# Performance work log

Hardware: AMD Instinct MI355X
Metric: run time of the kernel (lower is better)

The kernel has to match this reference:

```python
import jax, jax.numpy as jnp
import numpy as np


def setup_inputs() -> dict:
    key = jax.random.key(0)
    k1, k2 = jax.random.split(key)
    B, T = 16, 2048
    n_fft = 1024
    hop_length = 256
    win_length = 1024
    N = n_fft // 2 + 1  # 513 rfft bins
    spec_real = jax.random.normal(k1, (B, N, T), dtype=jnp.float32)
    spec_imag = jax.random.normal(k2, (B, N, T), dtype=jnp.float32)
    # periodic Hann window (torch.hann_window default)
    n = jnp.arange(win_length, dtype=jnp.float32)
    window = 0.5 * (1.0 - jnp.cos(2.0 * jnp.pi * n / win_length))
    return {
        "spec_real": spec_real,
        "spec_imag": spec_imag,
        "window": window,
        "n_fft": n_fft,
        "hop_length": hop_length,
        "win_length": win_length,
    }


def reference(spec_real, spec_imag, window, n_fft, hop_length, win_length):
    pad = (win_length - hop_length) // 2
    B, N, T = spec_real.shape
    spec = spec_real + 1j * spec_imag  # [B, N, T] complex
    # irfft along freq dim with 'backward' norm (jnp default): [B, n_fft, T]
    ifft = jnp.fft.irfft(spec, n=n_fft, axis=1)
    ifft = ifft * window[None, :, None]  # windowed frames
    L = (T - 1) * hop_length + win_length  # overlap-add output length
    # scatter indices: sample positions of each frame, shape [win_length, T]
    idx = jnp.arange(T)[None, :] * hop_length + jnp.arange(win_length)[:, None]
    y = jnp.zeros((B, L), dtype=ifft.dtype).at[:, idx].add(ifft)
    y = y[:, pad:L - pad]
    # window-squared envelope, same overlap-add pattern
    wsq = jnp.broadcast_to((window * window)[:, None], (win_length, T))
    env = jnp.zeros((L,), dtype=window.dtype).at[idx].add(wsq)[pad:L - pad]
    return y / env
```

## Files before the change

kernel.cpp:

```cpp
#include <hip/hip_runtime.h>

#define BB 16
#define TT 2048
#define NROW 513
#define HOP 256
#define OUTLB 524288
#define FTO 28
#define SPAN (FTO*HOP)
#define TILES 74
#define NCH 4
#define RZ 513

__device__ __forceinline__ int brev9(int k){ return (int)(__brev((unsigned)k)>>23); }
__device__ __forceinline__ int zidx(int f,int m){ return f*RZ + (m ^ ((m>>4)&28) ^ (f<<2)); }

__global__ __launch_bounds__(256,2) void istft_fused(
    const float* __restrict__ sr, const float* __restrict__ si,
    float* __restrict__ out)
{
  __shared__ float2 zc[8*RZ];
  __shared__ __align__(16) float2 ola[SPAN/2];
  __shared__ float2 ttab[256];

  const int tid  = threadIdx.x;
  const int b    = blockIdx.x / TILES;
  const int tile = blockIdx.x % TILES;
  const int L0   = tile*SPAN + 384;
  const int Tbase= tile*FTO - 2;

  { float s,c; __sincosf((float)tid*0.012271846303085130f,&s,&c); ttab[tid]=make_float2(c,s); }
  for (int i=tid;i<SPAN/2;i+=256) ola[i]=make_float2(0.f,0.f);

  const int f  = tid & 7;
  const int pp = tid >> 3;
  const float* srb = sr + (size_t)b*NROW*TT;
  const float* sib = si + (size_t)b*NROW*TT;

  for (int c = 0; c < NCH; ++c) {
    const int t  = Tbase + 8*c + f;
    const int tc = min(max(t,0),TT-1);
    const float msk = (t>=0 && t<TT) ? 1.f : 0.f;
    __syncthreads();

    for (int cc=0; cc<8; ++cc) {
      int k = cc*32 + pp;
      float ar = srb[(size_t)k*TT + tc]*msk;
      float ai = sib[(size_t)k*TT + tc]*msk;
      float br = srb[(size_t)(512-k)*TT + tc]*msk;
      float bi = sib[(size_t)(512-k)*TT + tc]*msk;
      if (k==0) {
        zc[zidx(f,0)] = make_float2(0.5f*(ar+br), 0.5f*(ar-br));
        float cr = srb[(size_t)256*TT + tc]*msk;
        float ci = sib[(size_t)256*TT + tc]*msk;
        zc[zidx(f,1)] = make_float2(cr,-ci);
      } else {
        float st,ct; __sincosf((float)k*0.006135923151542565f,&st,&ct);
        float Er=0.5f*(ar+br), Ei=0.5f*(ai-bi);
        float Dr=0.5f*(ar-br), Di=0.5f*(ai+bi);
        float Or=Dr*ct-Di*st,  Oi=Dr*st+Di*ct;
        zc[zidx(f,brev9(k))]     = make_float2(Er-Oi, Ei+Or);
        zc[zidx(f,brev9(512-k))] = make_float2(Er+Oi, Or-Ei);
      }
    }

    for (int st=0; st<4; ++st) {
      __syncthreads();
      const int h = 1<<(2*st);
      #pragma unroll
      for (int i=0;i<4;++i) {
        int q   = pp + 32*i;
        int ilo = q & (h-1);
        int base= ((q>>(2*st))<<(2*st+2)) + ilo;
        float2 w1 = ttab[ilo<<(8-2*st)];
        float2 w2 = ttab[ilo<<(7-2*st)];
        float2 e0=zc[zidx(f,base)],     e1=zc[zidx(f,base+h)];
        float2 e2=zc[zidx(f,base+2*h)], e3=zc[zidx(f,base+3*h)];
        float t1r=e1.x*w1.x-e1.y*w1.y, t1i=e1.x*w1.y+e1.y*w1.x;
        float t3r=e3.x*w1.x-e3.y*w1.y, t3i=e3.x*w1.y+e3.y*w1.x;
        float arr=e0.x+t1r, ari=e0.y+t1i, brr=e0.x-t1r, bri=e0.y-t1i;
        float crr=e2.x+t3r, cri=e2.y+t3i, drr=e2.x-t3r, dri=e2.y-t3i;
        float cwr=crr*w2.x-cri*w2.y, cwi=crr*w2.y+cri*w2.x;
        float dwr=drr*w2.x-dri*w2.y, dwi=drr*w2.y+dri*w2.x;
        zc[zidx(f,base)]     = make_float2(arr+cwr, ari+cwi);
        zc[zidx(f,base+2*h)] = make_float2(arr-cwr, ari-cwi);
        zc[zidx(f,base+h)]   = make_float2(brr-dwi, bri+dwr);
        zc[zidx(f,base+3*h)] = make_float2(brr+dwi, bri-dwr);
      }
    }
    __syncthreads();
    #pragma unroll
    for (int i=0;i<8;++i) {
      int q = pp + 32*i;
      float2 tw = ttab[q];
      float2 u = zc[zidx(f,q)], v = zc[zidx(f,q+256)];
      float tr=v.x*tw.x-v.y*tw.y, ti=v.x*tw.y+v.y*tw.x;
      zc[zidx(f,q)]     = make_float2(u.x+tr, u.y+ti);
      zc[zidx(f,q+256)] = make_float2(u.x-tr, u.y-ti);
    }

    for (int g=0; g<4; ++g) {
      __syncthreads();
      int slot = g + 4*(tid>>7);
      int tg   = Tbase + 8*c + slot;
      int offB = tg*HOP - L0;
      bool vt  = (tg>=0 && tg<TT);
      int mb   = tid & 127;
      #pragma unroll
      for (int i=0;i<4;++i) {
        int m = mb + 128*i;
        float2 v = zc[zidx(slot,m)];
        int j0 = 2*m;
        float w0 = 0.5f-0.5f*__cosf((float)j0    *0.006135923151542565f);
        float w1v= 0.5f-0.5f*__cosf((float)(j0+1)*0.006135923151542565f);
        int idx = offB + j0;
        if (vt && idx>=0 && idx<SPAN) {
          float2 o = ola[idx>>1];
          o.x += v.x*(1.f/512.f)*w0;
          o.y += v.y*(1.f/512.f)*w1v;
          ola[idx>>1] = o;
        }
      }
    }
  }
  __syncthreads();

  const bool edge = (tile==0)|(tile==TILES-1);
  float* outb = out + (size_t)b*OUTLB;
  for (int i=0;i<7;++i) {
    int i4 = tid + 256*i;
    int s  = 4*i4;
    int gs = tile*SPAN + s;
    if (gs < OUTLB) {
      float4 v = ((const float4*)ola)[i4];
      float r[4]={v.x,v.y,v.z,v.w};
      if (!edge) {
        #pragma unroll
        for(int e=0;e<4;++e) r[e] *= (2.f/3.f);
      } else {
        #pragma unroll
        for(int e=0;e<4;++e) {
          int l = L0 + s + e;
          int j0 = l & 255, tb = l >> 8;
          float env=0.f;
          #pragma unroll
          for (int mm=0;mm<4;++mm) {
            int t2 = tb-mm;
            if (t2>=0 && t2<TT) {
              float wv = 0.5f-0.5f*__cosf((float)(j0+256*mm)*0.006135923151542565f);
              env += wv*wv;
            }
          }
          r[e] /= env;
        }
      }
      *(float4*)(outb+gs) = make_float4(r[0],r[1],r[2],r[3]);
    }
  }
}

extern "C" void kernel_launch(void* const* d_in, const int* in_sizes, int n_in,
                              void* d_out, int out_size, void* d_ws, size_t ws_size,
                              hipStream_t stream) {
  const float* sr = (const float*)d_in[0];
  const float* si = (const float*)d_in[1];
  float* out = (float*)d_out;
  istft_fused<<<BB*TILES, 256, 0, stream>>>(sr, si, out);
}
```

Measured before the change: 260.1 us.

## Double block size and prefetch both frame chunks' spectra into registers per half

Threads per block go from 256 to 512, so each thread handles half the frequency rows per chunk. The four chunks become two halves. In each half, the loads for the second chunk are issued together with the first and held in registers, so global latency overlaps the first chunk's FFT and overlap-add. Post-twiddle sin/cos values are precomputed once per thread. The cost is higher register pressure and larger blocks, which may limit occupancy given the large shared-memory footprint.

New measurement: 262.0 us. Within noise of the previous version (+0.7%).

```diff
diff --git a/kernel.cpp b/kernel.cpp
--- a/kernel.cpp
+++ b/kernel.cpp
@@ -8,13 +8,12 @@
 #define FTO 28
 #define SPAN (FTO*HOP)
 #define TILES 74
-#define NCH 4
 #define RZ 513
 
 __device__ __forceinline__ int brev9(int k){ return (int)(__brev((unsigned)k)>>23); }
 __device__ __forceinline__ int zidx(int f,int m){ return f*RZ + (m ^ ((m>>4)&28) ^ (f<<2)); }
 
-__global__ __launch_bounds__(256,2) void istft_fused(
+__global__ __launch_bounds__(512,4) void istft_fused(
     const float* __restrict__ sr, const float* __restrict__ si,
     float* __restrict__ out)
 {
@@ -28,47 +27,45 @@
   const int L0   = tile*SPAN + 384;
   const int Tbase= tile*FTO - 2;
 
-  { float s,c; __sincosf((float)tid*0.012271846303085130f,&s,&c); ttab[tid]=make_float2(c,s); }
-  for (int i=tid;i<SPAN/2;i+=256) ola[i]=make_float2(0.f,0.f);
+  if (tid < 256) {
+    float s,c; __sincosf((float)tid*0.012271846303085130f,&s,&c);
+    ttab[tid]=make_float2(c,s);
+  }
+  for (int i=tid;i<SPAN/2;i+=512) ola[i]=make_float2(0.f,0.f);
 
   const int f  = tid & 7;
   const int pp = tid >> 3;
   const float* srb = sr + (size_t)b*NROW*TT;
   const float* sib = si + (size_t)b*NROW*TT;
 
-  for (int c = 0; c < NCH; ++c) {
-    const int t  = Tbase + 8*c + f;
-    const int tc = min(max(t,0),TT-1);
-    const float msk = (t>=0 && t<TT) ? 1.f : 0.f;
-    __syncthreads();
-
-    for (int cc=0; cc<8; ++cc) {
-      int k = cc*32 + pp;
-      float ar = srb[(size_t)k*TT + tc]*msk;
-      float ai = sib[(size_t)k*TT + tc]*msk;
-      float br = srb[(size_t)(512-k)*TT + tc]*msk;
-      float bi = sib[(size_t)(512-k)*TT + tc]*msk;
-      if (k==0) {
-        zc[zidx(f,0)] = make_float2(0.5f*(ar+br), 0.5f*(ar-br));
-        float cr = srb[(size_t)256*TT + tc]*msk;
-        float ci = sib[(size_t)256*TT + tc]*msk;
-        zc[zidx(f,1)] = make_float2(cr,-ci);
-      } else {
-        float st,ct; __sincosf((float)k*0.006135923151542565f,&st,&ct);
-        float Er=0.5f*(ar+br), Ei=0.5f*(ai-bi);
-        float Dr=0.5f*(ar-br), Di=0.5f*(ai+bi);
-        float Or=Dr*ct-Di*st,  Oi=Dr*st+Di*ct;
-        zc[zidx(f,brev9(k))]     = make_float2(Er-Oi, Ei+Or);
-        zc[zidx(f,brev9(512-k))] = make_float2(Er+Oi, Or-Ei);
-      }
-    }
-
-    for (int st=0; st<4; ++st) {
+  float ctw[4], stw[4];
+  #pragma unroll
+  for (int cc=0;cc<4;++cc){
+    __sincosf((float)(cc*64+pp)*0.006135923151542565f,&stw[cc],&ctw[cc]);
+  }
+
+  auto storeZ = [&](int cc, float ar,float ai,float br,float bi,float cr,float ci){
+    int k = cc*64+pp;
+    if (k==0){
+      zc[zidx(f,0)] = make_float2(0.5f*(ar+br), 0.5f*(ar-br));
+      zc[zidx(f,1)] = make_float2(cr, -ci);
+    } else {
+      float Er=0.5f*(ar+br), Ei=0.5f*(ai-bi);
+      float Dr=0.5f*(ar-br), Di=0.5f*(ai+bi);
+      float Or=Dr*ctw[cc]-Di*stw[cc], Oi=Dr*stw[cc]+Di*ctw[cc];
+      zc[zidx(f,brev9(k))]     = make_float2(Er-Oi, Ei+Or);
+      zc[zidx(f,brev9(512-k))] = make_float2(Er+Oi, Or-Ei);
+    }
+  };
+
+  auto do_fft = [&](){
+    #pragma unroll
+    for (int st=0; st<4; ++st){
       __syncthreads();
       const int h = 1<<(2*st);
       #pragma unroll
-      for (int i=0;i<4;++i) {
-        int q   = pp + 32*i;
+      for (int i=0;i<2;++i){
+        int q   = pp + 64*i;
         int ilo = q & (h-1);
         int base= ((q>>(2*st))<<(2*st+2)) + ilo;
         float2 w1 = ttab[ilo<<(8-2*st)];
@@ -89,31 +86,34 @@
     }
     __syncthreads();
     #pragma unroll
-    for (int i=0;i<8;++i) {
-      int q = pp + 32*i;
+    for (int i=0;i<4;++i){
+      int q = pp + 64*i;
       float2 tw = ttab[q];
       float2 u = zc[zidx(f,q)], v = zc[zidx(f,q+256)];
       float tr=v.x*tw.x-v.y*tw.y, ti=v.x*tw.y+v.y*tw.x;
       zc[zidx(f,q)]     = make_float2(u.x+tr, u.y+ti);
       zc[zidx(f,q+256)] = make_float2(u.x-tr, u.y-ti);
     }
-
-    for (int g=0; g<4; ++g) {
+  };
+
+  auto do_ola = [&](int chunkT){
+    #pragma unroll
+    for (int g=0; g<4; ++g){
       __syncthreads();
-      int slot = g + 4*(tid>>7);
-      int tg   = Tbase + 8*c + slot;
+      int slot = g + 4*(tid>>8);
+      int tg   = chunkT + slot;
       int offB = tg*HOP - L0;
       bool vt  = (tg>=0 && tg<TT);
-      int mb   = tid & 127;
+      int mbq  = tid & 255;
       #pragma unroll
-      for (int i=0;i<4;++i) {
-        int m = mb + 128*i;
+      for (int i=0;i<2;++i){
+        int m = mbq + 256*i;
         float2 v = zc[zidx(slot,m)];
         int j0 = 2*m;
         float w0 = 0.5f-0.5f*__cosf((float)j0    *0.006135923151542565f);
         float w1v= 0.5f-0.5f*__cosf((float)(j0+1)*0.006135923151542565f);
         int idx = offB + j0;
-        if (vt && idx>=0 && idx<SPAN) {
+        if (vt && idx>=0 && idx<SPAN){
           float2 o = ola[idx>>1];
           o.x += v.x*(1.f/512.f)*w0;
           o.y += v.y*(1.f/512.f)*w1v;
@@ -121,39 +121,88 @@
         }
       }
     }
+  };
+
+  for (int half=0; half<2; ++half){
+    const int c0  = 2*half;
+    const int ta  = Tbase + 8*c0 + f;
+    const int tb_ = ta + 8;
+    const int tca = min(max(ta ,0),TT-1);
+    const int tcb = min(max(tb_,0),TT-1);
+    const float ma  = (ta >=0 && ta <TT)?1.f:0.f;
+    const float mb2 = (tb_>=0 && tb_<TT)?1.f:0.f;
+
+    float sAr[4],sAi[4],sBr[4],sBi[4];
+    float sCr=0.f, sCi=0.f;
+
+    __syncthreads();
+    #pragma unroll
+    for (int cc=0;cc<4;++cc){
+      int k = cc*64+pp;
+      const float* pr  = srb + (size_t)k*TT;
+      const float* pi_ = sib + (size_t)k*TT;
+      const float* qr  = srb + (size_t)(512-k)*TT;
+      const float* qi  = sib + (size_t)(512-k)*TT;
+      float ar0=pr [tca], ar1=pr [tcb];
+      float ai0=pi_[tca], ai1=pi_[tcb];
+      float br0=qr [tca], br1=qr [tcb];
+      float bi0=qi [tca], bi1=qi [tcb];
+      sAr[cc]=ar1; sAi[cc]=ai1; sBr[cc]=br1; sBi[cc]=bi1;
+      float cr0=0.f, ci0=0.f;
+      if (cc==0 && pp==0){
+        const float* rr = srb + (size_t)256*TT;
+        const float* ri = sib + (size_t)256*TT;
+        cr0 = rr[tca]; sCr = rr[tcb];
+        ci0 = ri[tca]; sCi = ri[tcb];
+      }
+      storeZ(cc, ar0*ma, ai0*ma, br0*ma, bi0*ma, cr0*ma, ci0*ma);
+    }
+    do_fft();
+    do_ola(Tbase + 8*c0);
+
+    __syncthreads();
+    #pragma unroll
+    for (int cc=0;cc<4;++cc){
+      storeZ(cc, sAr[cc]*mb2, sAi[cc]*mb2, sBr[cc]*mb2, sBi[cc]*mb2, sCr*mb2, sCi*mb2);
+    }
+    do_fft();
+    do_ola(Tbase + 8*(c0+1));
   }
   __syncthreads();
 
   const bool edge = (tile==0)|(tile==TILES-1);
   float* outb = out + (size_t)b*OUTLB;
-  for (int i=0;i<7;++i) {
-    int i4 = tid + 256*i;
-    int s  = 4*i4;
-    int gs = tile*SPAN + s;
-    if (gs < OUTLB) {
-      float4 v = ((const float4*)ola)[i4];
-      float r[4]={v.x,v.y,v.z,v.w};
-      if (!edge) {
-        #pragma unroll
-        for(int e=0;e<4;++e) r[e] *= (2.f/3.f);
-      } else {
-        #pragma unroll
-        for(int e=0;e<4;++e) {
-          int l = L0 + s + e;
-          int j0 = l & 255, tb = l >> 8;
-          float env=0.f;
+  #pragma unroll
+  for (int i=0;i<4;++i){
+    int i4 = tid + 512*i;
+    if (i4 < SPAN/4){
+      int s  = 4*i4;
+      int gs = tile*SPAN + s;
+      if (gs < OUTLB){
+        float4 v = ((const float4*)ola)[i4];
+        float r[4]={v.x,v.y,v.z,v.w};
+        if (!edge){
           #pragma unroll
-          for (int mm=0;mm<4;++mm) {
-            int t2 = tb-mm;
-            if (t2>=0 && t2<TT) {
-              float wv = 0.5f-0.5f*__cosf((float)(j0+256*mm)*0.006135923151542565f);
-              env += wv*wv;
+          for(int e=0;e<4;++e) r[e] *= (2.f/3.f);
+        } else {
+          #pragma unroll
+          for(int e=0;e<4;++e){
+            int l = L0 + s + e;
+            int j0 = l & 255, tb = l >> 8;
+            float env=0.f;
+            #pragma unroll
+            for (int mm=0;mm<4;++mm){
+              int t2 = tb-mm;
+              if (t2>=0 && t2<TT){
+                float wv = 0.5f-0.5f*__cosf((float)(j0+256*mm)*0.006135923151542565f);
+                env += wv*wv;
+              }
             }
+            r[e] /= env;
           }
-          r[e] /= env;
         }
-      }
-      *(float4*)(outb+gs) = make_float4(r[0],r[1],r[2],r[3]);
+        *(float4*)(outb+gs) = make_float4(r[0],r[1],r[2],r[3]);
+      }
     }
   }
 }
@@ -164,5 +213,5 @@
   const float* sr = (const float*)d_in[0];
   const float* si = (const float*)d_in[1];
   float* out = (float*)d_out;
-  istft_fused<<<BB*TILES, 256, 0, stream>>>(sr, si, out);
+  istft_fused<<<BB*TILES, 512, 0, stream>>>(sr, si, out);
 }
```
